# Performance work log

Hardware: AMD Instinct MI355X
Metric: run time of the kernel (lower is better)

Reference implementation:

```python
import jax, jax.numpy as jnp
import numpy as np

NUM_CLASSES = 100
IN_DIM = 512
HID = 256
OUT_DIM = 512


def _xavier(key, shape):
    fan_in, fan_out = shape[1], shape[0]
    a = jnp.sqrt(6.0 / (fan_in + fan_out))
    return jax.random.uniform(key, shape, jnp.float32, -a, a)


def setup_inputs() -> dict:
    key = jax.random.key(0)
    ks = jax.random.split(key, 8)
    x = jax.random.normal(ks[0], (2048, IN_DIM), jnp.float32)
    # batched per-class expert params: [C, out, in] weights, [C, out] biases
    W1 = jax.vmap(lambda k: _xavier(k, (HID, IN_DIM)))(jax.random.split(ks[1], NUM_CLASSES))
    b1 = jnp.zeros((NUM_CLASSES, HID), jnp.float32)
    g1 = jnp.ones((NUM_CLASSES, HID), jnp.float32)
    be1 = jnp.zeros((NUM_CLASSES, HID), jnp.float32)
    W2 = jax.vmap(lambda k: _xavier(k, (HID, HID)))(jax.random.split(ks[2], NUM_CLASSES))
    b2 = jnp.zeros((NUM_CLASSES, HID), jnp.float32)
    g2 = jnp.ones((NUM_CLASSES, HID), jnp.float32)
    be2 = jnp.zeros((NUM_CLASSES, HID), jnp.float32)
    W3 = jax.vmap(lambda k: _xavier(k, (OUT_DIM, HID)))(jax.random.split(ks[3], NUM_CLASSES))
    b3 = jnp.zeros((NUM_CLASSES, OUT_DIM), jnp.float32)
    anchors = jax.random.normal(ks[4], (NUM_CLASSES, OUT_DIM), jnp.float32)
    return {"x": x, "W1": W1, "b1": b1, "g1": g1, "be1": be1,
            "W2": W2, "b2": b2, "g2": g2, "be2": be2,
            "W3": W3, "b3": b3, "anchors": anchors}


def _layernorm(h, g, b):
    mu = jnp.mean(h, axis=-1, keepdims=True)
    var = jnp.var(h, axis=-1, keepdims=True)
    return (h - mu) * jax.lax.rsqrt(var + 1e-5) * g + b


def reference(x, W1, b1, g1, be1, W2, b2, g2, be2, W3, b3, anchors):
    # all experts applied to all tokens (dense MoE); dropout is identity (eval)
    h = jnp.einsum('bi,chi->bch', x, W1) + b1  # [B, C, H]
    h = jax.nn.gelu(_layernorm(h, g1, be1), approximate=False)
    h = jnp.einsum('bch,cgh->bcg', h, W2) + b2
    h = jax.nn.gelu(_layernorm(h, g2, be2), approximate=False)
    t = jnp.einsum('bch,coh->bco', h, W3) + b3  # [B, C, O]
    t = t / jnp.linalg.norm(t, axis=-1, keepdims=True)
    a = anchors / jnp.linalg.norm(anchors, axis=-1, keepdims=True)  # [C, O]
    distances = jnp.linalg.norm(t - a[None, :, :], axis=-1)  # [B, C]
    similarities = jnp.sum(t * a[None, :, :], axis=-1)  # [B, C]
    routed = jnp.argmin(distances, axis=-1)
    return routed, distances, similarities
```

## Files before the change

kernel.cpp:

```cpp
#include <hip/hip_runtime.h>
#include <math.h>


#define NTOK 2048
#define NCLS 100
#define IND  512
#define HIDD 256
#define OUTD 512

typedef _Float16 half8 __attribute__((ext_vector_type(8)));
typedef __fp16 half2v __attribute__((ext_vector_type(2)));
typedef float f32x16 __attribute__((ext_vector_type(16)));

#define WSX_HALVES 2097152
#define CLS_STRIDE 655360
#define W2_OFF     262144
#define W3_OFF     393216
#define WS_NEED    ((size_t)(WSX_HALVES + 100 * CLS_STRIDE) * 2)

__device__ __forceinline__ unsigned h2u(half2v h) {
  union { half2v h; unsigned u; } t; t.h = h; return t.u;
}
__device__ __forceinline__ half8 u4h8(unsigned a, unsigned b, unsigned c, unsigned d) {
  union { unsigned u[4]; half8 h; } t; t.u[0] = a; t.u[1] = b; t.u[2] = c; t.u[3] = d; return t.h;
}
__device__ __forceinline__ f32x16 fzero16() {
  f32x16 z;
#pragma unroll
  for (int i = 0; i < 16; ++i) z[i] = 0.f;
  return z;
}

__device__ __forceinline__ void splitStore8(const float* __restrict__ src, _Float16* __restrict__ dst) {
  float4 f0 = *(const float4*)src, f1 = *(const float4*)(src + 4);
  float f[8] = {f0.x, f0.y, f0.z, f0.w, f1.x, f1.y, f1.z, f1.w};
  unsigned H[4], L[4];
#pragma unroll
  for (int i = 0; i < 4; ++i) {
    half2v ph = __builtin_amdgcn_cvt_pkrtz(f[2*i], f[2*i+1]);
    half2v pl = __builtin_amdgcn_cvt_pkrtz(f[2*i] - (float)ph[0], f[2*i+1] - (float)ph[1]);
    H[i] = h2u(ph); L[i] = h2u(pl);
  }
  *(half8*)dst = u4h8(H[0], H[1], H[2], H[3]);
  *(half8*)(dst + 512) = u4h8(L[0], L[1], L[2], L[3]);
}

extern "C" __global__ void __launch_bounds__(256)
split_x_k(const float* __restrict__ x, _Float16* __restrict__ wsx) {
  int tid = threadIdx.x, lane = tid & 63;
  int wid = blockIdx.x * 4 + (tid >> 6);
  int tokT = wid >> 5, kT = wid & 31;
  int l5 = lane & 31, g = lane >> 5;
  const float* src = x + ((size_t)(tokT * 32 + l5) * IND + kT * 16 + g * 8);
  _Float16* dst = wsx + (size_t)(tokT * 32 + kT) * 1024 + lane * 8;
  splitStore8(src, dst);
}

extern "C" __global__ void __launch_bounds__(256)
split_w_k(const float* __restrict__ W1, const float* __restrict__ W2, const float* __restrict__ W3,
          _Float16* __restrict__ wsw) {
  int tid = threadIdx.x, lane = tid & 63;
  int wid = blockIdx.x * 4 + (tid >> 6);
  int c = wid / 640, t = wid % 640;
  int l5 = lane & 31, g = lane >> 5;
  const float* src;
  if (t < 256) {
    src = W1 + ((size_t)(c * 256 + (t >> 5) * 32 + l5) * 512 + (t & 31) * 16 + g * 8);
  } else if (t < 384) {
    int tt = t - 256;
    src = W2 + ((size_t)(c * 256 + (tt >> 4) * 32 + l5) * 256 + (tt & 15) * 16 + g * 8);
  } else {
    int tt = t - 384;
    src = W3 + ((size_t)(c * 512 + (tt >> 4) * 32 + l5) * 256 + (tt & 15) * 16 + g * 8);
  }
  _Float16* dst = wsw + (size_t)(c * 640 + t) * 1024 + lane * 8;
  splitStore8(src, dst);
}

struct Frag8 { half8 hi, lo; };
struct FragSet { Frag8 a0, a1, b0, b1; };

__device__ __forceinline__ void ldFrag(Frag8& f, const _Float16* p) {
  f.hi = *(const half8*)(p);
  f.lo = *(const half8*)(p + 512);
}

template<int BS>
__device__ __forceinline__ void ldSet(FragSet& s, const _Float16* a0, const _Float16* a1,
                                      const _Float16* b0, const _Float16* b1, int k) {
  ldFrag(s.a0, a0 + (size_t)k * 1024);
  ldFrag(s.a1, a1 + (size_t)k * 1024);
  ldFrag(s.b0, b0 + (size_t)k * BS);
  ldFrag(s.b1, b1 + (size_t)k * BS);
}

#define MFMA(A, B, C) __builtin_amdgcn_mfma_f32_32x32x16_f16((A), (B), (C), 0, 0, 0)

__device__ __forceinline__ void mmSet(const FragSet& s, f32x16 acc[2][2]) {
  acc[0][0] = MFMA(s.a0.hi, s.b0.hi, acc[0][0]);
  acc[0][0] = MFMA(s.a0.hi, s.b0.lo, acc[0][0]);
  acc[0][0] = MFMA(s.a0.lo, s.b0.hi, acc[0][0]);
  acc[0][1] = MFMA(s.a0.hi, s.b1.hi, acc[0][1]);
  acc[0][1] = MFMA(s.a0.hi, s.b1.lo, acc[0][1]);
  acc[0][1] = MFMA(s.a0.lo, s.b1.hi, acc[0][1]);
  acc[1][0] = MFMA(s.a1.hi, s.b0.hi, acc[1][0]);
  acc[1][0] = MFMA(s.a1.hi, s.b0.lo, acc[1][0]);
  acc[1][0] = MFMA(s.a1.lo, s.b0.hi, acc[1][0]);
  acc[1][1] = MFMA(s.a1.hi, s.b1.hi, acc[1][1]);
  acc[1][1] = MFMA(s.a1.hi, s.b1.lo, acc[1][1]);
  acc[1][1] = MFMA(s.a1.lo, s.b1.hi, acc[1][1]);
}

template<int NK, int BS>
__device__ __forceinline__ void kloop(const _Float16* __restrict__ a0, const _Float16* __restrict__ a1,
                                      const _Float16* b0, const _Float16* b1, f32x16 acc[2][2]) {
  FragSet X, Y;
  ldSet<BS>(X, a0, a1, b0, b1, 0);
#pragma unroll 1
  for (int kp = 0; kp < NK / 2 - 1; ++kp) {
    ldSet<BS>(Y, a0, a1, b0, b1, 2 * kp + 1);
    mmSet(X, acc);
    ldSet<BS>(X, a0, a1, b0, b1, 2 * kp + 2);
    mmSet(Y, acc);
  }
  ldSet<BS>(Y, a0, a1, b0, b1, NK - 1);
  mmSet(X, acc);
  mmSet(Y, acc);
}

__device__ __forceinline__ void lnGeluFrag(f32x16 acc[2][2],
                                           const float* __restrict__ bias, const float* __restrict__ gam,
                                           const float* __restrict__ bet, int cb,
                                           _Float16* sH, float (*sStat)[64][2],
                                           int w, int l5, int g, int lane) {
#pragma unroll
  for (int mt = 0; mt < 2; ++mt) {
    int ob = cb + (2 * w + mt) * 32 + (g ? 4 : 0);
#pragma unroll
    for (int r = 0; r < 16; ++r) {
      int rr = (r & 3) + 8 * (r >> 2);
      float bb = bias[ob + rr];
      acc[mt][0][r] += bb;
      acc[mt][1][r] += bb;
    }
  }
  float s0 = 0.f, q0 = 0.f, s1 = 0.f, q1 = 0.f;
#pragma unroll
  for (int mt = 0; mt < 2; ++mt)
#pragma unroll
    for (int r = 0; r < 16; ++r) {
      float v0 = acc[mt][0][r]; s0 += v0; q0 += v0 * v0;
      float v1 = acc[mt][1][r]; s1 += v1; q1 += v1 * v1;
    }
  s0 += __shfl_xor(s0, 32, 64); q0 += __shfl_xor(q0, 32, 64);
  s1 += __shfl_xor(s1, 32, 64); q1 += __shfl_xor(q1, 32, 64);
  if (lane < 32) {
    sStat[w][l5][0] = s0;      sStat[w][l5][1] = q0;
    sStat[w][l5 + 32][0] = s1; sStat[w][l5 + 32][1] = q1;
  }
  __syncthreads();
  float S0 = 0.f, Q0 = 0.f, S1 = 0.f, Q1 = 0.f;
#pragma unroll
  for (int ww = 0; ww < 4; ++ww) {
    S0 += sStat[ww][l5][0];      Q0 += sStat[ww][l5][1];
    S1 += sStat[ww][l5 + 32][0]; Q1 += sStat[ww][l5 + 32][1];
  }
  float mu0 = S0 * (1.f / HIDD), var0 = Q0 * (1.f / HIDD) - mu0 * mu0;
  float rs0 = rsqrtf(var0 + 1e-5f);
  float mu1 = S1 * (1.f / HIDD), var1 = Q1 * (1.f / HIDD) - mu1 * mu1;
  float rs1 = rsqrtf(var1 + 1e-5f);
#pragma unroll
  for (int mt = 0; mt < 2; ++mt) {
    int ob = cb + (2 * w + mt) * 32 + (g ? 4 : 0);
#pragma unroll
    for (int r = 0; r < 16; ++r) {
      int rr = (r & 3) + 8 * (r >> 2);
      float gm = gam[ob + rr], bt = bet[ob + rr];
      float v0 = (acc[mt][0][r] - mu0) * rs0 * gm + bt;
      acc[mt][0][r] = 0.5f * v0 * (1.f + erff(v0 * 0.70710678118654752f));
      float v1 = (acc[mt][1][r] - mu1) * rs1 * gm + bt;
      acc[mt][1][r] = 0.5f * v1 * (1.f + erff(v1 * 0.70710678118654752f));
    }
  }
#pragma unroll
  for (int mt = 0; mt < 2; ++mt) {
#pragma unroll
    for (int nt = 0; nt < 2; ++nt) {
      unsigned P[8], L[8];
#pragma unroll
      for (int i = 0; i < 8; ++i) {
        float a0 = acc[mt][nt][2 * i], a1 = acc[mt][nt][2 * i + 1];
        half2v ph = __builtin_amdgcn_cvt_pkrtz(a0, a1);
        half2v pl = __builtin_amdgcn_cvt_pkrtz(a0 - (float)ph[0], a1 - (float)ph[1]);
        P[i] = h2u(ph); L[i] = h2u(pl);
      }
#pragma unroll
      for (int kt = 0; kt < 2; ++kt) {
        unsigned s0h = g ? P[4 * kt + 0] : P[4 * kt + 2];
        unsigned s1h = g ? P[4 * kt + 1] : P[4 * kt + 3];
        unsigned s0l = g ? L[4 * kt + 0] : L[4 * kt + 2];
        unsigned s1l = g ? L[4 * kt + 1] : L[4 * kt + 3];
        unsigned r0h = __shfl_xor(s0h, 32, 64);
        unsigned r1h = __shfl_xor(s1h, 32, 64);
        unsigned r0l = __shfl_xor(s0l, 32, 64);
        unsigned r1l = __shfl_xor(s1l, 32, 64);
        unsigned hv0 = g ? r0h : P[4 * kt + 0];
        unsigned hv1 = g ? r1h : P[4 * kt + 1];
        unsigned hv2 = g ? P[4 * kt + 2] : r0h;
        unsigned hv3 = g ? P[4 * kt + 3] : r1h;
        unsigned lv0 = g ? r0l : L[4 * kt + 0];
        unsigned lv1 = g ? r1l : L[4 * kt + 1];
        unsigned lv2 = g ? L[4 * kt + 2] : r0l;
        unsigned lv3 = g ? L[4 * kt + 3] : r1l;
        int kT = 4 * w + 2 * mt + kt;
        _Float16* dst = sH + (size_t)((kT * 2 + nt) * 2) * 512 + lane * 8;
        *(half8*)dst = u4h8(hv0, hv1, hv2, hv3);
        *(half8*)(dst + 512) = u4h8(lv0, lv1, lv2, lv3);
      }
    }
  }
  __syncthreads();
}

extern "C" __global__ void __launch_bounds__(256, 2)
moe_f16(const _Float16* __restrict__ wsx, const _Float16* __restrict__ wsw,
        const float* __restrict__ b1, const float* __restrict__ g1, const float* __restrict__ be1,
        const float* __restrict__ b2, const float* __restrict__ g2, const float* __restrict__ be2,
        const float* __restrict__ b3, const float* __restrict__ anchors,
        float* __restrict__ out_dist, float* __restrict__ out_sim) {
  __shared__ _Float16 sH[32768];
  __shared__ float sStat[4][64][2];

  const int tid = threadIdx.x;
  const int lane = tid & 63, w = tid >> 6;
  const int l5 = lane & 31, g = lane >> 5;

  const int p0 = blockIdx.x;
  const int lg = (p0 & 7) * 400 + (p0 >> 3);
  const int c = lg >> 5;
  const int tokT2 = lg & 31;

  {
    float a0 = anchors[c * OUTD + tid];
    float a1 = anchors[c * OUTD + 256 + tid];
    float aa = a0 * a0 + a1 * a1;
#pragma unroll
    for (int m = 1; m <= 32; m <<= 1) aa += __shfl_xor(aa, m, 64);
    if (lane == 0) sStat[w][0][0] = aa;
  }
  __syncthreads();
  const float rinv = rsqrtf(sStat[0][0][0] + sStat[1][0][0] + sStat[2][0][0] + sStat[3][0][0]);
  __syncthreads();

  const _Float16* wc = wsw + (size_t)c * CLS_STRIDE + lane * 8;
  const _Float16* xB0 = wsx + (size_t)((tokT2 * 2 + 0) * 32) * 1024 + lane * 8;
  const _Float16* xB1 = wsx + (size_t)((tokT2 * 2 + 1) * 32) * 1024 + lane * 8;
  const _Float16* sB0 = sH + 0 * 1024 + lane * 8;
  const _Float16* sB1 = sH + 1 * 1024 + lane * 8;

  f32x16 acc[2][2];

  acc[0][0] = fzero16(); acc[0][1] = fzero16(); acc[1][0] = fzero16(); acc[1][1] = fzero16();
  kloop<32, 1024>(wc + (size_t)(2 * w + 0) * 32 * 1024,
                  wc + (size_t)(2 * w + 1) * 32 * 1024, xB0, xB1, acc);
  lnGeluFrag(acc, b1, g1, be1, c * HIDD, sH, sStat, w, l5, g, lane);

  acc[0][0] = fzero16(); acc[0][1] = fzero16(); acc[1][0] = fzero16(); acc[1][1] = fzero16();
  kloop<16, 2048>(wc + W2_OFF + (size_t)(2 * w + 0) * 16 * 1024,
                  wc + W2_OFF + (size_t)(2 * w + 1) * 16 * 1024, sB0, sB1, acc);
  lnGeluFrag(acc, b2, g2, be2, c * HIDD, sH, sStat, w, l5, g, lane);

  float pdot0 = 0.f, psq0 = 0.f, pdot1 = 0.f, psq1 = 0.f;
#pragma unroll 1
  for (int p = 0; p < 2; ++p) {
    acc[0][0] = fzero16(); acc[0][1] = fzero16(); acc[1][0] = fzero16(); acc[1][1] = fzero16();
    kloop<16, 2048>(wc + W3_OFF + (size_t)(8 * p + 2 * w + 0) * 16 * 1024,
                    wc + W3_OFF + (size_t)(8 * p + 2 * w + 1) * 16 * 1024, sB0, sB1, acc);
#pragma unroll
    for (int mt = 0; mt < 2; ++mt) {
      int ob = c * OUTD + (8 * p + 2 * w + mt) * 32 + (g ? 4 : 0);
#pragma unroll
      for (int r = 0; r < 16; ++r) {
        int rr = (r & 3) + 8 * (r >> 2);
        float bb = b3[ob + rr];
        float av = anchors[ob + rr] * rinv;
        float t0 = acc[mt][0][r] + bb;
        pdot0 = fmaf(t0, av, pdot0); psq0 = fmaf(t0, t0, psq0);
        float t1 = acc[mt][1][r] + bb;
        pdot1 = fmaf(t1, av, pdot1); psq1 = fmaf(t1, t1, psq1);
      }
    }
  }
  pdot0 += __shfl_xor(pdot0, 32, 64); psq0 += __shfl_xor(psq0, 32, 64);
  pdot1 += __shfl_xor(pdot1, 32, 64); psq1 += __shfl_xor(psq1, 32, 64);
  if (lane < 32) {
    sStat[w][l5][0] = pdot0;      sStat[w][l5][1] = psq0;
    sStat[w][l5 + 32][0] = pdot1; sStat[w][l5 + 32][1] = psq1;
  }
  __syncthreads();
  if (tid < 64) {
    float dd = 0.f, qq = 0.f;
#pragma unroll
    for (int ww = 0; ww < 4; ++ww) { dd += sStat[ww][tid][0]; qq += sStat[ww][tid][1]; }
    float s = dd * rsqrtf(qq);
    float d = sqrtf(fmaxf(2.f - 2.f * s, 0.f));
    int t = tokT2 * 64 + tid;
    out_dist[(size_t)t * NCLS + c] = d;
    out_sim[(size_t)t * NCLS + c] = s;
  }
}

extern "C" __global__ void __launch_bounds__(256)
argmin_routed(const float* __restrict__ dist, float* __restrict__ routed) {
  int b = blockIdx.x * blockDim.x + threadIdx.x;
  if (b >= NTOK) return;
  const float* d = dist + (size_t)b * NCLS;
  float best = d[0];
  int bi = 0;
#pragma unroll 1
  for (int cc = 1; cc < NCLS; ++cc) {
    float v = d[cc];
    if (v < best) { best = v; bi = cc; }
  }
  routed[b] = (float)bi;
}

#define BT   64
#define KT   16
#define SA   68
#define SWS  260

__device__ __forceinline__ float4 ld4(const float* p) { return *(const float4*)p; }

__device__ __forceinline__ void loadW4(float4 wr[4], const float* __restrict__ gp, int k0) {
#pragma unroll
  for (int i = 0; i < 4; ++i) wr[i] = ld4(gp + k0 + 4 * i);
}

__device__ __forceinline__ void storeW4(float* sW, const float4 wr[4], int t) {
#pragma unroll
  for (int i = 0; i < 4; ++i) {
    sW[(4 * i + 0) * SWS + t] = wr[i].x;
    sW[(4 * i + 1) * SWS + t] = wr[i].y;
    sW[(4 * i + 2) * SWS + t] = wr[i].z;
    sW[(4 * i + 3) * SWS + t] = wr[i].w;
  }
}

__device__ __forceinline__ void storeX4(float* sX, const float4 xr, int xtok, int xkh) {
  sX[(xkh * 4 + 0) * SA + xtok] = xr.x;
  sX[(xkh * 4 + 1) * SA + xtok] = xr.y;
  sX[(xkh * 4 + 2) * SA + xtok] = xr.z;
  sX[(xkh * 4 + 3) * SA + xtok] = xr.w;
}

__device__ __forceinline__ void fma_chunk(const float* __restrict__ A, const float* __restrict__ sW,
                                          int ty8, int o_lo, int o_hi, float acc[8][8]) {
#pragma unroll
  for (int k = 0; k < KT; ++k) {
    const float* a = A + k * SA + ty8;
    float4 t0 = ld4(a);
    float4 t1 = ld4(a + 4);
    const float* wp = sW + k * SWS;
    float4 w0 = ld4(wp + o_lo);
    float4 w1 = ld4(wp + o_hi);
    float tv[8] = {t0.x, t0.y, t0.z, t0.w, t1.x, t1.y, t1.z, t1.w};
    float wv[8] = {w0.x, w0.y, w0.z, w0.w, w1.x, w1.y, w1.z, w1.w};
#pragma unroll
    for (int j = 0; j < 8; ++j)
#pragma unroll
      for (int i = 0; i < 8; ++i)
        acc[j][i] = fmaf(tv[j], wv[i], acc[j][i]);
  }
}

template <int NC>
__device__ __forceinline__ void gemm_phase(const float* __restrict__ gRow, const float* __restrict__ A,
                                           float* sW, int tid, int ty8, int o_lo, int o_hi,
                                           float acc[8][8]) {
  float4 wr[4];
  loadW4(wr, gRow, 0);
  __syncthreads();
  storeW4(sW, wr, tid);
  __syncthreads();
#pragma unroll 1
  for (int kc = 0; kc < NC; ++kc) {
    if (kc + 1 < NC) loadW4(wr, gRow, (kc + 1) * KT);
    fma_chunk(A + kc * KT * SA, sW, ty8, o_lo, o_hi, acc);
    if (kc + 1 < NC) {
      __syncthreads();
      storeW4(sW, wr, tid);
      __syncthreads();
    }
  }
}

__device__ __forceinline__ void gemm_phase1(const float* __restrict__ gWrow, const float* __restrict__ gXrow,
                                            float* sW, float* sX, int tid, int xtok, int xkh,
                                            int ty8, int o_lo, int o_hi, float acc[8][8]) {
  float4 wr[4];
  float4 xr;
  loadW4(wr, gWrow, 0);
  xr = ld4(gXrow);
  __syncthreads();
  storeW4(sW, wr, tid);
  storeX4(sX, xr, xtok, xkh);
  __syncthreads();
#pragma unroll 1
  for (int kc = 0; kc < IND / KT; ++kc) {
    if (kc + 1 < IND / KT) {
      loadW4(wr, gWrow, (kc + 1) * KT);
      xr = ld4(gXrow + (kc + 1) * KT);
    }
    fma_chunk(sX, sW, ty8, o_lo, o_hi, acc);
    if (kc + 1 < IND / KT) {
      __syncthreads();
      storeW4(sW, wr, tid);
      storeX4(sX, xr, xtok, xkh);
      __syncthreads();
    }
  }
}

__device__ __forceinline__ void ln_gelu_store(float acc[8][8], const float* __restrict__ bias,
                                              const float* __restrict__ gam, const float* __restrict__ bet,
                                              int cb, float* sHd, int ty8, int o_lo, int o_hi) {
  float4 q0 = ld4(bias + cb + o_lo), q1 = ld4(bias + cb + o_hi);
  float bv[8] = {q0.x, q0.y, q0.z, q0.w, q1.x, q1.y, q1.z, q1.w};
  float4 g0 = ld4(gam + cb + o_lo), g1q = ld4(gam + cb + o_hi);
  float gv[8] = {g0.x, g0.y, g0.z, g0.w, g1q.x, g1q.y, g1q.z, g1q.w};
  float4 e0 = ld4(bet + cb + o_lo), e1 = ld4(bet + cb + o_hi);
  float ev[8] = {e0.x, e0.y, e0.z, e0.w, e1.x, e1.y, e1.z, e1.w};

  float sum[8], ssq[8];
#pragma unroll
  for (int j = 0; j < 8; ++j) {
    float s = 0.f, q = 0.f;
#pragma unroll
    for (int i = 0; i < 8; ++i) {
      float v = acc[j][i] + bv[i];
      acc[j][i] = v;
      s += v;
      q += v * v;
    }
    sum[j] = s;
    ssq[j] = q;
  }
#pragma unroll
  for (int m = 1; m <= 16; m <<= 1) {
#pragma unroll
    for (int j = 0; j < 8; ++j) {
      sum[j] += __shfl_xor(sum[j], m, 64);
      ssq[j] += __shfl_xor(ssq[j], m, 64);
    }
  }
#pragma unroll
  for (int j = 0; j < 8; ++j) {
    float mu = sum[j] * (1.f / HIDD);
    float var = ssq[j] * (1.f / HIDD) - mu * mu;
    float rs = rsqrtf(var + 1e-5f);
#pragma unroll
    for (int i = 0; i < 8; ++i) {
      float v = (acc[j][i] - mu) * rs * gv[i] + ev[i];
      acc[j][i] = 0.5f * v * (1.f + erff(v * 0.70710678118654752f));
    }
  }
#pragma unroll
  for (int i = 0; i < 8; ++i) {
    int o = (i < 4) ? (o_lo + i) : (o_hi + (i - 4));
    float4 pq0, pq1;
    pq0.x = acc[0][i]; pq0.y = acc[1][i]; pq0.z = acc[2][i]; pq0.w = acc[3][i];
    pq1.x = acc[4][i]; pq1.y = acc[5][i]; pq1.z = acc[6][i]; pq1.w = acc[7][i];
    *(float4*)(sHd + o * SA + ty8) = pq0;
    *(float4*)(sHd + o * SA + ty8 + 4) = pq1;
  }
}

extern "C" __global__ void __launch_bounds__(256)
moe_fused_f32(const float* __restrict__ x, const float* __restrict__ W1, const float* __restrict__ b1,
              const float* __restrict__ g1, const float* __restrict__ be1,
              const float* __restrict__ W2, const float* __restrict__ b2,
              const float* __restrict__ g2, const float* __restrict__ be2,
              const float* __restrict__ W3, const float* __restrict__ b3,
              const float* __restrict__ anchors,
              float* __restrict__ out_dist, float* __restrict__ out_sim) {
  __shared__ __align__(16) float sW[KT * SWS];
  __shared__ __align__(16) float sX[KT * SA];
  __shared__ __align__(16) float sHd[HIDD * SA];
  __shared__ float sRed[4];

  const int tid = threadIdx.x;
  const int tx = tid & 31, ty = tid >> 5;
  const int ty8 = ty * 8;
  const int o_lo = 4 * tx, o_hi = 128 + 4 * tx;
  const int c = blockIdx.y;
  const int tb = blockIdx.x * BT;

  {
    float v0 = anchors[c * OUTD + tid];
    float v1 = anchors[c * OUTD + 256 + tid];
    float aa = v0 * v0 + v1 * v1;
#pragma unroll
    for (int m = 1; m <= 32; m <<= 1) aa += __shfl_xor(aa, m, 64);
    if ((tid & 63) == 0) sRed[tid >> 6] = aa;
  }
  __syncthreads();
  const float rinv = rsqrtf(sRed[0] + sRed[1] + sRed[2] + sRed[3]);

  float acc[8][8];

#pragma unroll
  for (int j = 0; j < 8; ++j)
#pragma unroll
    for (int i = 0; i < 8; ++i) acc[j][i] = 0.f;

  gemm_phase1(W1 + (size_t)(c * HIDD + tid) * IND,
              x + (size_t)(tb + (tid & 63)) * IND + (tid >> 6) * 4,
              sW, sX, tid, tid & 63, tid >> 6, ty8, o_lo, o_hi, acc);
  ln_gelu_store(acc, b1, g1, be1, c * HIDD, sHd, ty8, o_lo, o_hi);

#pragma unroll
  for (int j = 0; j < 8; ++j)
#pragma unroll
    for (int i = 0; i < 8; ++i) acc[j][i] = 0.f;

  gemm_phase<HIDD / KT>(W2 + (size_t)(c * HIDD + tid) * HIDD, sHd, sW, tid, ty8, o_lo, o_hi, acc);
  __syncthreads();
  ln_gelu_store(acc, b2, g2, be2, c * HIDD, sHd, ty8, o_lo, o_hi);

  float pdot[8], psq[8];
#pragma unroll
  for (int j = 0; j < 8; ++j) { pdot[j] = 0.f; psq[j] = 0.f; }

#pragma unroll 1
  for (int p = 0; p < 2; ++p) {
#pragma unroll
    for (int j = 0; j < 8; ++j)
#pragma unroll
      for (int i = 0; i < 8; ++i) acc[j][i] = 0.f;

    gemm_phase<HIDD / KT>(W3 + (size_t)(c * OUTD + p * 256 + tid) * HIDD, sHd, sW, tid, ty8, o_lo, o_hi, acc);

    const int ob = c * OUTD + p * 256;
    float4 q0 = ld4(b3 + ob + o_lo), q1 = ld4(b3 + ob + o_hi);
    float bv[8] = {q0.x, q0.y, q0.z, q0.w, q1.x, q1.y, q1.z, q1.w};
    float4 a0 = ld4(anchors + ob + o_lo), a1 = ld4(anchors + ob + o_hi);
    float av[8] = {a0.x * rinv, a0.y * rinv, a0.z * rinv, a0.w * rinv,
                   a1.x * rinv, a1.y * rinv, a1.z * rinv, a1.w * rinv};
#pragma unroll
    for (int j = 0; j < 8; ++j)
#pragma unroll
      for (int i = 0; i < 8; ++i) {
        float t = acc[j][i] + bv[i];
        pdot[j] = fmaf(t, av[i], pdot[j]);
        psq[j] = fmaf(t, t, psq[j]);
      }
  }

#pragma unroll
  for (int m = 1; m <= 16; m <<= 1) {
#pragma unroll
    for (int j = 0; j < 8; ++j) {
      pdot[j] += __shfl_xor(pdot[j], m, 64);
      psq[j] += __shfl_xor(psq[j], m, 64);
    }
  }
  if (tx < 8) {
    float pd = 0.f, pq = 1.f;
#pragma unroll
    for (int j = 0; j < 8; ++j)
      if (tx == j) { pd = pdot[j]; pq = psq[j]; }
    const int b = tb + ty8 + tx;
    float s = pd * rsqrtf(pq);
    float d = sqrtf(fmaxf(2.f - 2.f * s, 0.f));
    out_dist[(size_t)b * NCLS + c] = d;
    out_sim[(size_t)b * NCLS + c] = s;
  }
}

extern "C" void kernel_launch(void* const* d_in, const int* in_sizes, int n_in,
                              void* d_out, int out_size, void* d_ws, size_t ws_size,
                              hipStream_t stream) {
  const float* x = (const float*)d_in[0];
  const float* W1 = (const float*)d_in[1];
  const float* b1 = (const float*)d_in[2];
  const float* g1 = (const float*)d_in[3];
  const float* be1 = (const float*)d_in[4];
  const float* W2 = (const float*)d_in[5];
  const float* b2 = (const float*)d_in[6];
  const float* g2 = (const float*)d_in[7];
  const float* be2 = (const float*)d_in[8];
  const float* W3 = (const float*)d_in[9];
  const float* b3 = (const float*)d_in[10];
  const float* anchors = (const float*)d_in[11];

  float* out = (float*)d_out;
  float* out_routed = out;
  float* out_dist = out + NTOK;
  float* out_sim = out + NTOK + NTOK * NCLS;

  if (ws_size >= WS_NEED) {
    _Float16* wsh = (_Float16*)d_ws;
    split_x_k<<<512, 256, 0, stream>>>(x, wsh);
    split_w_k<<<16000, 256, 0, stream>>>(W1, W2, W3, wsh + WSX_HALVES);
    moe_f16<<<3200, 256, 0, stream>>>(wsh, wsh + WSX_HALVES,
                                      b1, g1, be1, b2, g2, be2, b3, anchors,
                                      out_dist, out_sim);
  } else {
    dim3 grid(NTOK / BT, NCLS);
    moe_fused_f32<<<grid, 256, 0, stream>>>(x, W1, b1, g1, be1, W2, b2, g2, be2, W3, b3,
                                            anchors, out_dist, out_sim);
  }
  argmin_routed<<<NTOK / 256, 256, 0, stream>>>(out_dist, out_routed);
}
```

Before: 715.0 us.

## Stage layer-1 token fragments into LDS via async global_load_lds double buffering

Layer-1 GEMM token operands are no longer read by every wave straight from global memory. They are staged chunk by chunk into double-buffered shared memory with direct global-to-LDS loads, overlapped with the MFMA work on the previous chunk. The split kernels are also rewritten so each wave reads contiguous rows of x and W, giving coalesced fp32 loads while producing the same fragment layout. The trade-off is extra barriers and vmcnt waits per chunk, and possible LDS occupancy pressure.

```diff
diff --git a/kernel.cpp b/kernel.cpp
--- a/kernel.cpp
+++ b/kernel.cpp
@@ -31,6 +31,12 @@
   return z;
 }
 
+__device__ __forceinline__ void gload_lds16(const void* gsrc, void* ldst) {
+  __builtin_amdgcn_global_load_lds(
+      (const __attribute__((address_space(1))) unsigned int*)gsrc,
+      (__attribute__((address_space(3))) unsigned int*)ldst, 16, 0, 0);
+}
+
 __device__ __forceinline__ void splitStore8(const float* __restrict__ src, _Float16* __restrict__ dst) {
   float4 f0 = *(const float4*)src, f1 = *(const float4*)(src + 4);
   float f[8] = {f0.x, f0.y, f0.z, f0.w, f1.x, f1.y, f1.z, f1.w};
@@ -48,11 +54,10 @@
 extern "C" __global__ void __launch_bounds__(256)
 split_x_k(const float* __restrict__ x, _Float16* __restrict__ wsx) {
   int tid = threadIdx.x, lane = tid & 63;
-  int wid = blockIdx.x * 4 + (tid >> 6);
-  int tokT = wid >> 5, kT = wid & 31;
-  int l5 = lane & 31, g = lane >> 5;
-  const float* src = x + ((size_t)(tokT * 32 + l5) * IND + kT * 16 + g * 8);
-  _Float16* dst = wsx + (size_t)(tokT * 32 + kT) * 1024 + lane * 8;
+  int rr = blockIdx.x * 4 + (tid >> 6);
+  const float* src = x + (size_t)rr * IND + lane * 8;
+  int kT = lane >> 1, g = lane & 1;
+  _Float16* dst = wsx + (size_t)((rr >> 5) * 32 + kT) * 1024 + (g * 32 + (rr & 31)) * 8;
   splitStore8(src, dst);
 }
 
@@ -61,20 +66,30 @@
           _Float16* __restrict__ wsw) {
   int tid = threadIdx.x, lane = tid & 63;
   int wid = blockIdx.x * 4 + (tid >> 6);
-  int c = wid / 640, t = wid % 640;
-  int l5 = lane & 31, g = lane >> 5;
-  const float* src;
-  if (t < 256) {
-    src = W1 + ((size_t)(c * 256 + (t >> 5) * 32 + l5) * 512 + (t & 31) * 16 + g * 8);
-  } else if (t < 384) {
-    int tt = t - 256;
-    src = W2 + ((size_t)(c * 256 + (tt >> 4) * 32 + l5) * 256 + (tt & 15) * 16 + g * 8);
+  int l5 = lane & 31;
+  if (wid < 25600) {
+    int c = wid >> 8, rr = wid & 255;
+    const float* src = W1 + ((size_t)(c * 256 + rr) * 512 + lane * 8);
+    int kT = lane >> 1, g = lane & 1;
+    _Float16* dst = wsw + (size_t)(c * 640 + (rr >> 5) * 32 + kT) * 1024 + (g * 32 + (rr & 31)) * 8;
+    splitStore8(src, dst);
+  } else if (wid < 38400) {
+    int t = wid - 25600;
+    int R = 2 * t + (lane >> 5);
+    int c = R >> 8, rr = R & 255;
+    const float* src = W2 + ((size_t)(c * 256 + rr) * 256 + l5 * 8);
+    int kT = l5 >> 1, g = l5 & 1;
+    _Float16* dst = wsw + (size_t)(c * 640 + 256 + (rr >> 5) * 16 + kT) * 1024 + (g * 32 + (rr & 31)) * 8;
+    splitStore8(src, dst);
   } else {
-    int tt = t - 384;
-    src = W3 + ((size_t)(c * 512 + (tt >> 4) * 32 + l5) * 256 + (tt & 15) * 16 + g * 8);
-  }
-  _Float16* dst = wsw + (size_t)(c * 640 + t) * 1024 + lane * 8;
-  splitStore8(src, dst);
+    int t = wid - 38400;
+    int R = 2 * t + (lane >> 5);
+    int c = R >> 9, rr = R & 511;
+    const float* src = W3 + ((size_t)(c * 512 + rr) * 256 + l5 * 8);
+    int kT = l5 >> 1, g = l5 & 1;
+    _Float16* dst = wsw + (size_t)(c * 640 + 384 + (rr >> 5) * 16 + kT) * 1024 + (g * 32 + (rr & 31)) * 8;
+    splitStore8(src, dst);
+  }
 }
 
 struct Frag8 { half8 hi, lo; };
@@ -92,6 +107,14 @@
   ldFrag(s.a1, a1 + (size_t)k * 1024);
   ldFrag(s.b0, b0 + (size_t)k * BS);
   ldFrag(s.b1, b1 + (size_t)k * BS);
+}
+
+__device__ __forceinline__ void ldSetL(FragSet& s, const _Float16* a0, const _Float16* a1,
+                                       const _Float16* bb, int kk) {
+  ldFrag(s.a0, a0 + (size_t)kk * 1024);
+  ldFrag(s.a1, a1 + (size_t)kk * 1024);
+  ldFrag(s.b0, bb + kk * 2048);
+  ldFrag(s.b1, bb + kk * 2048 + 1024);
 }
 
 #define MFMA(A, B, C) __builtin_amdgcn_mfma_f32_32x32x16_f16((A), (B), (C), 0, 0, 0)
@@ -126,6 +149,35 @@
   ldSet<BS>(Y, a0, a1, b0, b1, NK - 1);
   mmSet(X, acc);
   mmSet(Y, acc);
+}
+
+__device__ __forceinline__ void chunk8(const _Float16* __restrict__ a0, const _Float16* __restrict__ a1,
+                                       const _Float16* bb, f32x16 acc[2][2]) {
+  FragSet X, Y;
+  ldSetL(X, a0, a1, bb, 0);
+  ldSetL(Y, a0, a1, bb, 1);
+#pragma unroll
+  for (int kp = 0; kp < 3; ++kp) {
+    mmSet(X, acc);
+    ldSetL(X, a0, a1, bb, 2 * kp + 2);
+    mmSet(Y, acc);
+    ldSetL(Y, a0, a1, bb, 2 * kp + 3);
+  }
+  mmSet(X, acc);
+  mmSet(Y, acc);
+}
+
+__device__ __forceinline__ void stage_chunk(const _Float16* __restrict__ xs0,
+                                            const _Float16* __restrict__ xs1,
+                                            _Float16* buf, int cch, int w, int lane) {
+#pragma unroll
+  for (int i = 0; i < 8; ++i) {
+    int slot = w * 8 + i;
+    int kT = slot >> 2, tok = (slot >> 1) & 1, part = slot & 1;
+    const _Float16* src = (tok ? xs1 : xs0) + (size_t)(cch * 8 + kT) * 1024 + part * 512 + lane * 8;
+    _Float16* dst = buf + (kT * 2 + tok) * 1024 + part * 512;
+    gload_lds16(src, dst);
+  }
 }
 
 __device__ __forceinline__ void lnGeluFrag(f32x16 acc[2][2],
@@ -240,6 +292,11 @@
   const int c = lg >> 5;
   const int tokT2 = lg & 31;
 
+  const _Float16* xs0 = wsx + (size_t)((tokT2 * 2 + 0) * 32) * 1024;
+  const _Float16* xs1 = wsx + (size_t)((tokT2 * 2 + 1) * 32) * 1024;
+
+  stage_chunk(xs0, xs1, sH, 0, w, lane);
+
   {
     float a0 = anchors[c * OUTD + tid];
     float a1 = anchors[c * OUTD + 256 + tid];
@@ -250,19 +307,26 @@
   }
   __syncthreads();
   const float rinv = rsqrtf(sStat[0][0][0] + sStat[1][0][0] + sStat[2][0][0] + sStat[3][0][0]);
+  asm volatile("s_waitcnt vmcnt(0)" ::: "memory");
   __syncthreads();
 
   const _Float16* wc = wsw + (size_t)c * CLS_STRIDE + lane * 8;
-  const _Float16* xB0 = wsx + (size_t)((tokT2 * 2 + 0) * 32) * 1024 + lane * 8;
-  const _Float16* xB1 = wsx + (size_t)((tokT2 * 2 + 1) * 32) * 1024 + lane * 8;
+  const _Float16* wA0 = wc + (size_t)(2 * w + 0) * 32 * 1024;
+  const _Float16* wA1 = wc + (size_t)(2 * w + 1) * 32 * 1024;
   const _Float16* sB0 = sH + 0 * 1024 + lane * 8;
   const _Float16* sB1 = sH + 1 * 1024 + lane * 8;
 
   f32x16 acc[2][2];
 
   acc[0][0] = fzero16(); acc[0][1] = fzero16(); acc[1][0] = fzero16(); acc[1][1] = fzero16();
-  kloop<32, 1024>(wc + (size_t)(2 * w + 0) * 32 * 1024,
-                  wc + (size_t)(2 * w + 1) * 32 * 1024, xB0, xB1, acc);
+#pragma unroll 1
+  for (int cch = 0; cch < 4; ++cch) {
+    if (cch < 3) stage_chunk(xs0, xs1, sH + ((cch + 1) & 1) * 16384, cch + 1, w, lane);
+    chunk8(wA0 + (size_t)cch * 8 * 1024, wA1 + (size_t)cch * 8 * 1024,
+           sH + (cch & 1) * 16384 + lane * 8, acc);
+    asm volatile("s_waitcnt vmcnt(0)" ::: "memory");
+    __syncthreads();
+  }
   lnGeluFrag(acc, b1, g1, be1, c * HIDD, sH, sStat, w, l5, g, lane);
 
   acc[0][0] = fzero16(); acc[0][1] = fzero16(); acc[1][0] = fzero16(); acc[1][1] = fzero16();
```

After: 738.4 us. +3.3%, slower.

## Deepen k-loop prefetch to triple buffering and coalesce split-kernel reads

Applied to the files above, without the earlier changes.

The MFMA k-loop now keeps three fragment sets in flight instead of two, issuing loads three steps ahead so more global-load latency is hidden behind matrix ops, at the cost of more VGPRs and clamped redundant loads at the tail. The split kernels for x and the weights are remapped so each wave reads contiguous rows (coalesced global reads) and scatters into the same tiled fp16 hi/lo layout. The higher register pressure may reduce occupancy.

```diff
diff --git a/kernel.cpp b/kernel.cpp
--- a/kernel.cpp
+++ b/kernel.cpp
@@ -48,11 +48,10 @@
 extern "C" __global__ void __launch_bounds__(256)
 split_x_k(const float* __restrict__ x, _Float16* __restrict__ wsx) {
   int tid = threadIdx.x, lane = tid & 63;
-  int wid = blockIdx.x * 4 + (tid >> 6);
-  int tokT = wid >> 5, kT = wid & 31;
-  int l5 = lane & 31, g = lane >> 5;
-  const float* src = x + ((size_t)(tokT * 32 + l5) * IND + kT * 16 + g * 8);
-  _Float16* dst = wsx + (size_t)(tokT * 32 + kT) * 1024 + lane * 8;
+  int rr = blockIdx.x * 4 + (tid >> 6);
+  const float* src = x + (size_t)rr * IND + lane * 8;
+  int kT = lane >> 1, g = lane & 1;
+  _Float16* dst = wsx + (size_t)((rr >> 5) * 32 + kT) * 1024 + (g * 32 + (rr & 31)) * 8;
   splitStore8(src, dst);
 }
 
@@ -61,20 +60,30 @@
           _Float16* __restrict__ wsw) {
   int tid = threadIdx.x, lane = tid & 63;
   int wid = blockIdx.x * 4 + (tid >> 6);
-  int c = wid / 640, t = wid % 640;
-  int l5 = lane & 31, g = lane >> 5;
-  const float* src;
-  if (t < 256) {
-    src = W1 + ((size_t)(c * 256 + (t >> 5) * 32 + l5) * 512 + (t & 31) * 16 + g * 8);
-  } else if (t < 384) {
-    int tt = t - 256;
-    src = W2 + ((size_t)(c * 256 + (tt >> 4) * 32 + l5) * 256 + (tt & 15) * 16 + g * 8);
+  int l5 = lane & 31;
+  if (wid < 25600) {
+    int c = wid >> 8, rr = wid & 255;
+    const float* src = W1 + ((size_t)(c * 256 + rr) * 512 + lane * 8);
+    int kT = lane >> 1, g = lane & 1;
+    _Float16* dst = wsw + (size_t)(c * 640 + (rr >> 5) * 32 + kT) * 1024 + (g * 32 + (rr & 31)) * 8;
+    splitStore8(src, dst);
+  } else if (wid < 38400) {
+    int t = wid - 25600;
+    int R = 2 * t + (lane >> 5);
+    int c = R >> 8, rr = R & 255;
+    const float* src = W2 + ((size_t)(c * 256 + rr) * 256 + l5 * 8);
+    int kT = l5 >> 1, g = l5 & 1;
+    _Float16* dst = wsw + (size_t)(c * 640 + 256 + (rr >> 5) * 16 + kT) * 1024 + (g * 32 + (rr & 31)) * 8;
+    splitStore8(src, dst);
   } else {
-    int tt = t - 384;
-    src = W3 + ((size_t)(c * 512 + (tt >> 4) * 32 + l5) * 256 + (tt & 15) * 16 + g * 8);
-  }
-  _Float16* dst = wsw + (size_t)(c * 640 + t) * 1024 + lane * 8;
-  splitStore8(src, dst);
+    int t = wid - 38400;
+    int R = 2 * t + (lane >> 5);
+    int c = R >> 9, rr = R & 511;
+    const float* src = W3 + ((size_t)(c * 512 + rr) * 256 + l5 * 8);
+    int kT = l5 >> 1, g = l5 & 1;
+    _Float16* dst = wsw + (size_t)(c * 640 + 384 + (rr >> 5) * 16 + kT) * 1024 + (g * 32 + (rr & 31)) * 8;
+    splitStore8(src, dst);
+  }
 }
 
 struct Frag8 { half8 hi, lo; };
@@ -114,18 +123,25 @@
 template<int NK, int BS>
 __device__ __forceinline__ void kloop(const _Float16* __restrict__ a0, const _Float16* __restrict__ a1,
                                       const _Float16* b0, const _Float16* b1, f32x16 acc[2][2]) {
-  FragSet X, Y;
-  ldSet<BS>(X, a0, a1, b0, b1, 0);
+  FragSet S0, S1, S2;
+  ldSet<BS>(S0, a0, a1, b0, b1, 0);
+  ldSet<BS>(S1, a0, a1, b0, b1, 1);
+  ldSet<BS>(S2, a0, a1, b0, b1, 2);
 #pragma unroll 1
-  for (int kp = 0; kp < NK / 2 - 1; ++kp) {
-    ldSet<BS>(Y, a0, a1, b0, b1, 2 * kp + 1);
-    mmSet(X, acc);
-    ldSet<BS>(X, a0, a1, b0, b1, 2 * kp + 2);
-    mmSet(Y, acc);
-  }
-  ldSet<BS>(Y, a0, a1, b0, b1, NK - 1);
-  mmSet(X, acc);
-  mmSet(Y, acc);
+  for (int kb = 0; kb < NK / 3; ++kb) {
+    int k = 3 * kb;
+    int k3 = (k + 3 < NK) ? k + 3 : NK - 1;
+    int k4 = (k + 4 < NK) ? k + 4 : NK - 1;
+    int k5 = (k + 5 < NK) ? k + 5 : NK - 1;
+    mmSet(S0, acc);
+    ldSet<BS>(S0, a0, a1, b0, b1, k3);
+    mmSet(S1, acc);
+    ldSet<BS>(S1, a0, a1, b0, b1, k4);
+    mmSet(S2, acc);
+    ldSet<BS>(S2, a0, a1, b0, b1, k5);
+  }
+  if (NK % 3 >= 1) mmSet(S0, acc);
+  if (NK % 3 >= 2) mmSet(S1, acc);
 }
 
 __device__ __forceinline__ void lnGeluFrag(f32x16 acc[2][2],
```

After: 748.5 us. +4.7%, slower.
